# Optimization experiments

Measured on AMD Instinct MI355X. Metric: run time of the kernel, lower is better.

The kernel has to match this reference:

```python
import jax, jax.numpy as jnp
import numpy as np

N = 16384   # nodes = batch(4) * 64*64 grid
E = 32768   # edges per edge set
L = 32      # LATENT_DIMS
D = 2       # DEPTH (message-passing layers per GNOBlock)
KD = 64     # KERNEL_DIMS
TIN = 10    # TIME_STEPS_IN

def gelu(x):
    return jax.nn.gelu(x, approximate=False)  # torch F.gelu default (erf)

def setup_inputs() -> dict:
    key = jax.random.key(0)
    ks = iter(jax.random.split(key, 64))
    def nrm(shape, s=0.1):
        return jax.random.normal(next(ks), shape, dtype=jnp.float32) * s
    def ridx():
        return jax.random.randint(next(ks), (2, E), 0, N)
    inp = {
        'nodes': nrm((N, TIN), 1.0),
        'grid': jax.random.uniform(next(ks), (N, 2), dtype=jnp.float32),
    }
    for nm in ['11', '12', '22', '23', '33', '32', '21']:
        inp[f'edge_index_{nm}'] = ridx()
    for nm in ['11', '12', '22', '23', '33', '32', '21']:
        inp[f'edge_attr_{nm}'] = nrm((E, 5), 1.0)
    inp['batch_size'] = 4
    inp['image_size'] = 64
    # projector MLP: in_dims=TIN+2 -> hidden L//2 -> L
    inp['proj_w1'] = nrm((TIN + 2, L // 2)); inp['proj_b1'] = jnp.zeros((L // 2,), jnp.float32)
    inp['proj_w2'] = nrm((L // 2, L));       inp['proj_b2'] = jnp.zeros((L,), jnp.float32)
    # decoder MLP: L -> L//2 -> 1
    inp['dec_w1'] = nrm((L, L // 2)); inp['dec_b1'] = jnp.zeros((L // 2,), jnp.float32)
    inp['dec_w2'] = nrm((L // 2, 1)); inp['dec_b2'] = jnp.zeros((1,), jnp.float32)
    # 7 GNOBlocks x D layers: edge kernel MLP (5 -> KD -> L*L) + node linear (L -> L)
    inp['kw1'] = nrm((7, D, 5, KD));      inp['kb1'] = jnp.zeros((7, D, KD), jnp.float32)
    inp['kw2'] = nrm((7, D, KD, L * L));  inp['kb2'] = jnp.zeros((7, D, L * L), jnp.float32)
    inp['lw'] = nrm((7, D, L, L));        inp['lb'] = jnp.zeros((7, D, L), jnp.float32)
    return inp

def _mlp(x, w1, b1, w2, b2):
    return gelu(x @ w1 + b1) @ w2 + b2

def _gno_block(i, x, eidx, eattr, kw1, kb1, kw2, kb2, lw, lb):
    src, dst = eidx[0], eidx[1]
    n = x.shape[0]
    deg = jax.ops.segment_sum(jnp.ones_like(dst, x.dtype), dst, num_segments=n)
    inv_deg = jnp.where(deg > 0, 1.0 / jnp.maximum(deg, 1.0), 0.0)[:, None]
    for d in range(kw1.shape[1]):
        # edge-conditioned kernel: [E, L, L]
        k = _mlp(eattr, kw1[i, d], kb1[i, d], kw2[i, d], kb2[i, d]).reshape(-1, x.shape[1], x.shape[1])
        msg = jnp.einsum('eio,ei->eo', k, x[src])            # gather + per-edge matvec
        agg = jax.ops.segment_sum(msg, dst, num_segments=n) * inv_deg  # scatter-mean
        x = gelu(x @ lw[i, d] + lb[i, d] + agg)              # root linear + activation
    return x

def reference(nodes, grid, edge_index_11, edge_index_12, edge_index_22, edge_index_23,
              edge_index_33, edge_index_32, edge_index_21, edge_attr_11, edge_attr_12,
              edge_attr_22, edge_attr_23, edge_attr_33, edge_attr_32, edge_attr_21,
              batch_size, image_size, proj_w1, proj_b1, proj_w2, proj_b2,
              dec_w1, dec_b1, dec_w2, dec_b2, kw1, kb1, kw2, kb2, lw, lb):
    x = jnp.concatenate([nodes, grid], axis=-1)
    x = gelu(_mlp(x, proj_w1, proj_b1, proj_w2, proj_b2))
    # block param index order matches init order: k11,k22,k33,k12,k23,k32,k21
    n11 = _gno_block(0, x, edge_index_11, edge_attr_11, kw1, kb1, kw2, kb2, lw, lb)
    n12 = _gno_block(3, x, edge_index_12, edge_attr_12, kw1, kb1, kw2, kb2, lw, lb)
    n22 = _gno_block(1, n12, edge_index_22, edge_attr_22, kw1, kb1, kw2, kb2, lw, lb)
    n23 = _gno_block(4, n12, edge_index_23, edge_attr_23, kw1, kb1, kw2, kb2, lw, lb)
    n33 = _gno_block(2, n23, edge_index_33, edge_attr_33, kw1, kb1, kw2, kb2, lw, lb)
    n32 = _gno_block(5, n33, edge_index_32, edge_attr_32, kw1, kb1, kw2, kb2, lw, lb)
    n21 = _gno_block(6, n32 + n22, edge_index_21, edge_attr_21, kw1, kb1, kw2, kb2, lw, lb)
    out = _mlp(n21 + n11, dec_w1, dec_b1, dec_w2, dec_b2)
    return out
```

## Files before the change

kernel.cpp:

```cpp
#include <hip/hip_runtime.h>

#define Nn 16384
#define Ee 32768
#define NL (Nn * 32)

typedef _Float16 hf16;
typedef _Float16 half8 __attribute__((ext_vector_type(8)));
typedef float f32x16 __attribute__((ext_vector_type(16)));

__device__ __forceinline__ float gelu_f(float x) {
    return 0.5f * x * (1.0f + erff(x * 0.7071067811865476f));
}

__device__ __forceinline__ f32x16 zero16() {
    f32x16 v;
#pragma unroll
    for (int r = 0; r < 16; ++r) v[r] = 0.0f;
    return v;
}

struct EPtrs { const int* p[7]; };
struct EA14  { const float* p[14]; };

__global__ __launch_bounds__(256) void proj_kernel(
    const float* __restrict__ nodes, const float* __restrict__ grid2,
    const float* __restrict__ w1, const float* __restrict__ b1,
    const float* __restrict__ w2, const float* __restrict__ b2,
    float* __restrict__ x0, int* __restrict__ deg_i, int* __restrict__ cursor)
{
    const int n = blockIdx.x * 256 + threadIdx.x;
    float in[12];
#pragma unroll
    for (int j = 0; j < 10; ++j) in[j] = nodes[n * 10 + j];
    in[10] = grid2[n * 2 + 0];
    in[11] = grid2[n * 2 + 1];
    float h[16];
#pragma unroll
    for (int j = 0; j < 16; ++j) {
        float a = b1[j];
#pragma unroll
        for (int i = 0; i < 12; ++i) a = fmaf(in[i], w1[i * 16 + j], a);
        h[j] = gelu_f(a);
    }
#pragma unroll
    for (int o = 0; o < 32; ++o) {
        float a = b2[o];
#pragma unroll
        for (int j = 0; j < 16; ++j) a = fmaf(h[j], w2[j * 32 + o], a);
        x0[(size_t)n * 32 + o] = gelu_f(a);
    }
#pragma unroll
    for (int s = 0; s < 7; ++s) { deg_i[s * Nn + n] = 0; cursor[s * Nn + n] = 0; }
}

__global__ __launch_bounds__(256) void count_deg_kernel(EPtrs ei, int* __restrict__ deg_i)
{
    const int t = blockIdx.x * 256 + threadIdx.x;
    const int s = t >> 15;
    const int e = t & (Ee - 1);
    const int dst = ei.p[s][Ee + e];
    atomicAdd(&deg_i[s * Nn + dst], 1);
}

__global__ __launch_bounds__(256) void scan_kernel(const int* __restrict__ deg_i,
                                                   int* __restrict__ off)
{
    const int s = blockIdx.x;
    const int t = threadIdx.x;
    const int* d = deg_i + (size_t)s * Nn;
    int* o = off + (size_t)s * (Nn + 1);
    int local[64];
    int sum = 0;
#pragma unroll
    for (int j = 0; j < 64; ++j) { local[j] = d[t * 64 + j]; sum += local[j]; }
    __shared__ int ps[256];
    ps[t] = sum;
    __syncthreads();
    for (int st = 1; st < 256; st <<= 1) {
        int v = (t >= st) ? ps[t - st] : 0;
        __syncthreads();
        ps[t] += v;
        __syncthreads();
    }
    int base = (t > 0) ? ps[t - 1] : 0;
#pragma unroll
    for (int j = 0; j < 64; ++j) { o[t * 64 + j] = base; base += local[j]; }
    if (t == 255) o[Nn] = base;
}

__global__ __launch_bounds__(256) void rank_kernel(EPtrs ei, const int* __restrict__ off,
                                                   int* __restrict__ cursor,
                                                   int* __restrict__ eord,
                                                   int* __restrict__ srcS)
{
    const int t = blockIdx.x * 256 + threadIdx.x;
    const int s = t >> 15;
    const int e = t & (Ee - 1);
    const int dst = ei.p[s][Ee + e];
    const int r = off[(size_t)s * (Nn + 1) + dst] + atomicAdd(&cursor[s * Nn + dst], 1);
    eord[(size_t)s * Ee + r] = e;
    srcS[(size_t)s * Ee + r] = ei.p[s][e];
}

__global__ __launch_bounds__(256) void wprep_kernel(const float* __restrict__ kw2,
                                                    hf16* __restrict__ Wpack)
{
    const int id = blockIdx.x >> 5;
    const int nt = blockIdx.x & 31;
    const int t = threadIdx.x;
    const int ks = t >> 6, lane = t & 63;
    const float* kw2l = kw2 + (size_t)id * 65536;
    half8 vh, vl;
#pragma unroll
    for (int j = 0; j < 8; ++j) {
        const int k = ks * 16 + (lane >> 5) * 8 + j;
        const float v = kw2l[(size_t)k * 1024 + (lane & 31) * 32 + nt];
        const hf16 h = (hf16)v;
        vh[j] = h;
        vl[j] = (hf16)((v - (float)h) * 1024.0f);
    }
    half8* dst = (half8*)(Wpack + ((size_t)(id * 32 + nt) * 8 + ks * 2) * 512);
    dst[0 * 64 + lane] = vh;
    dst[1 * 64 + lane] = vl;
}

__global__ __launch_bounds__(256) void hprep_kernel(
    EA14 ea, const float* __restrict__ kw1, const float* __restrict__ kb1,
    hf16* __restrict__ Hpack)
{
    const int b = blockIdx.x;
    const int u = b >> 8;
    const int tgrp = b & 255;
    const int t = threadIdx.x, l = t & 63, wv = t >> 6;
    const int tile = tgrp * 4 + wv;
    const int eg = tile * 32 + (l & 31);
    const float* kw1u = kw1 + (size_t)u * 320;
    const float* kb1u = kb1 + (size_t)u * 64;
    float ea5[5];
#pragma unroll
    for (int j = 0; j < 5; ++j) ea5[j] = ea.p[u][(size_t)eg * 5 + j];
    half8* hp = (half8*)Hpack;
#pragma unroll
    for (int ks = 0; ks < 4; ++ks) {
        half8 vh, vl;
#pragma unroll
        for (int j = 0; j < 8; ++j) {
            const int k = ks * 16 + (l >> 5) * 8 + j;
            float pre = kb1u[k];
#pragma unroll
            for (int q = 0; q < 5; ++q) pre = fmaf(ea5[q], kw1u[q * 64 + k], pre);
            const float H = gelu_f(pre);
            const hf16 hv = (hf16)H;
            vh[j] = hv;
            vl[j] = (hf16)((H - (float)hv) * 1024.0f);
        }
        const size_t fb = ((size_t)(u * 1024 + tile) * 8 + ks * 2) * 64;
        hp[fb + l] = vh;
        hp[fb + 64 + l] = vl;
    }
}

__global__ __launch_bounds__(256) void gemm_kernel(
    const float* __restrict__ xa, const float* __restrict__ xb,
    const int* __restrict__ esrc,
    const hf16* __restrict__ HpackU,
    const hf16* __restrict__ WpackL,
    float* __restrict__ msgS)
{
    const int lb = ((blockIdx.x & 7) << 7) + (blockIdx.x >> 3);
    const int eblk = lb >> 2;
    const int qid = lb & 3;
    const int t = threadIdx.x, l = t & 63, wv = t >> 6;
    const int tile = eblk * 4 + wv;

    const half8* hp = (const half8*)HpackU + (size_t)tile * 8 * 64;
    half8 Hh[4], Hl[4];
#pragma unroll
    for (int ks = 0; ks < 4; ++ks) {
        Hh[ks] = hp[(ks * 2 + 0) * 64 + l];
        Hl[ks] = hp[(ks * 2 + 1) * 64 + l];
    }

    const int hi = l >> 5;
    const int el = tile * 32 + (l & 31);
    const int src = esrc[el];
    float xsr[16];
#pragma unroll
    for (int c = 0; c < 4; ++c) {
        float4 v = *reinterpret_cast<const float4*>(xa + (size_t)src * 32 + c * 8 + hi * 4);
        if (xb) {
            float4 u = *reinterpret_cast<const float4*>(xb + (size_t)src * 32 + c * 8 + hi * 4);
            v.x += u.x; v.y += u.y; v.z += u.z; v.w += u.w;
        }
        xsr[c * 4 + 0] = v.x; xsr[c * 4 + 1] = v.y;
        xsr[c * 4 + 2] = v.z; xsr[c * 4 + 3] = v.w;
    }

    float4 p4;
    const hf16* wbase = WpackL + (size_t)qid * 8 * 4096;

#define LOADW(TT, WH, WL) { \
    const half8* wp = (const half8*)(wbase + (size_t)(TT) * 4096); \
    _Pragma("unroll") for (int ks = 0; ks < 4; ++ks) { \
        WH[ks] = wp[(ks * 2 + 0) * 64 + l]; \
        WL[ks] = wp[(ks * 2 + 1) * 64 + l]; } }

#define COMPUTE(TT, WH, WL) { \
    f32x16 ah = zero16(), ax = zero16(); \
    _Pragma("unroll") for (int ks = 0; ks < 4; ++ks) { \
        ah = __builtin_amdgcn_mfma_f32_32x32x16_f16(WH[ks], Hh[ks], ah, 0, 0, 0); \
        ax = __builtin_amdgcn_mfma_f32_32x32x16_f16(WL[ks], Hh[ks], ax, 0, 0, 0); \
        ax = __builtin_amdgcn_mfma_f32_32x32x16_f16(WH[ks], Hl[ks], ax, 0, 0, 0); } \
    float ph = 0.0f, px = 0.0f; \
    _Pragma("unroll") for (int r = 0; r < 16; ++r) { \
        ph = fmaf(ah[r], xsr[r], ph); px = fmaf(ax[r], xsr[r], px); } \
    float p = fmaf(px, 9.765625e-4f, ph); \
    p += __shfl_xor(p, 32); \
    p4[(TT) & 3] = p; \
    if (((TT) & 3) == 3 && l < 32) \
        *reinterpret_cast<float4*>(msgS + (size_t)el * 32 + qid * 8 + ((TT) - 3)) = p4; }

    half8 WhA[4], WlA[4], WhB[4], WlB[4];
    LOADW(0, WhA, WlA)
#pragma unroll
    for (int g = 0; g < 4; ++g) {
        LOADW(2 * g + 1, WhB, WlB)
        COMPUTE(2 * g, WhA, WlA)
        if (g < 3) LOADW(2 * g + 2, WhA, WlA)
        COMPUTE(2 * g + 1, WhB, WlB)
    }
#undef LOADW
#undef COMPUTE
}

__global__ __launch_bounds__(256) void node_update_kernel(
    const float* __restrict__ xa, const float* __restrict__ xb,
    float* __restrict__ xout, const float* __restrict__ msgS,
    const int* __restrict__ off, const int* __restrict__ eord,
    const int* __restrict__ srcS,
    const float* __restrict__ lw, const float* __restrict__ lb,
    const float* __restrict__ kb2l)
{
    __shared__ float lwS[1024];
    __shared__ float kbS[1024];
#pragma unroll
    for (int c = 0; c < 4; ++c) {
        lwS[threadIdx.x + 256 * c] = lw[threadIdx.x + 256 * c];
        kbS[threadIdx.x + 256 * c] = kb2l[threadIdx.x + 256 * c];
    }
    __syncthreads();

    const int g = blockIdx.x * 256 + threadIdx.x;
    const int n = g >> 3;
    const int q = g & 7;

    const int b = off[n], e = off[n + 1];
    float sum[4];
    float xsum[32];
#pragma unroll
    for (int oo = 0; oo < 4; ++oo) sum[oo] = 0.0f;
#pragma unroll
    for (int i = 0; i < 32; ++i) xsum[i] = 0.0f;
    for (int j = b; j < e; ++j) {
        const int eid = eord[j];
        const float4 m0 = *reinterpret_cast<const float4*>(msgS + (size_t)eid * 32 + q * 4);
        sum[0] += m0.x; sum[1] += m0.y; sum[2] += m0.z; sum[3] += m0.w;
        const int src = srcS[j];
#pragma unroll
        for (int c = 0; c < 8; ++c) {
            float4 v = *reinterpret_cast<const float4*>(xa + (size_t)src * 32 + c * 4);
            if (xb) {
                float4 u = *reinterpret_cast<const float4*>(xb + (size_t)src * 32 + c * 4);
                v.x += u.x; v.y += u.y; v.z += u.z; v.w += u.w;
            }
            xsum[c * 4 + 0] += v.x; xsum[c * 4 + 1] += v.y;
            xsum[c * 4 + 2] += v.z; xsum[c * 4 + 3] += v.w;
        }
    }
    const float inv = (e > b) ? 1.0f / (float)(e - b) : 0.0f;
    float acc[4];
#pragma unroll
    for (int oo = 0; oo < 4; ++oo) acc[oo] = fmaf(sum[oo], inv, lb[q * 4 + oo]);

    float row[32];
#pragma unroll
    for (int i = 0; i < 32; i += 4) {
        float4 v = *reinterpret_cast<const float4*>(xa + (size_t)n * 32 + i);
        if (xb) {
            float4 u = *reinterpret_cast<const float4*>(xb + (size_t)n * 32 + i);
            v.x += u.x; v.y += u.y; v.z += u.z; v.w += u.w;
        }
        row[i + 0] = v.x; row[i + 1] = v.y; row[i + 2] = v.z; row[i + 3] = v.w;
    }
#pragma unroll
    for (int i = 0; i < 32; ++i) {
        const float xi = row[i];
        const float xm = xsum[i] * inv;
#pragma unroll
        for (int oo = 0; oo < 4; ++oo) {
            acc[oo] = fmaf(xi, lwS[i * 32 + q * 4 + oo], acc[oo]);
            acc[oo] = fmaf(xm, kbS[i * 32 + q * 4 + oo], acc[oo]);
        }
    }
    float4 o0;
    o0.x = gelu_f(acc[0]); o0.y = gelu_f(acc[1]);
    o0.z = gelu_f(acc[2]); o0.w = gelu_f(acc[3]);
    *reinterpret_cast<float4*>(xout + (size_t)n * 32 + q * 4) = o0;
}

__global__ __launch_bounds__(256) void decode_kernel(
    const float* __restrict__ a, const float* __restrict__ b,
    const float* __restrict__ w1, const float* __restrict__ b1,
    const float* __restrict__ w2, const float* __restrict__ b2,
    float* __restrict__ out)
{
    const int n = blockIdx.x * 256 + threadIdx.x;
    float s[32];
#pragma unroll
    for (int i = 0; i < 32; ++i) s[i] = a[(size_t)n * 32 + i] + b[(size_t)n * 32 + i];
    float acc = b2[0];
#pragma unroll
    for (int j = 0; j < 16; ++j) {
        float h = b1[j];
#pragma unroll
        for (int i = 0; i < 32; ++i) h = fmaf(s[i], w1[i * 16 + j], h);
        acc = fmaf(gelu_f(h), w2[j], acc);
    }
    out[n] = acc;
}

extern "C" void kernel_launch(void* const* d_in, const int* in_sizes, int n_in,
                              void* d_out, int out_size, void* d_ws, size_t ws_size,
                              hipStream_t stream)
{
    const float* nodes = (const float*)d_in[0];
    const float* grid2 = (const float*)d_in[1];
    const int* ei[7];
    const float* ea[7];
    for (int s = 0; s < 7; ++s) {
        ei[s] = (const int*)d_in[2 + s];
        ea[s] = (const float*)d_in[9 + s];
    }
    const float* pw1 = (const float*)d_in[18];
    const float* pb1 = (const float*)d_in[19];
    const float* pw2 = (const float*)d_in[20];
    const float* pb2 = (const float*)d_in[21];
    const float* dw1 = (const float*)d_in[22];
    const float* db1 = (const float*)d_in[23];
    const float* dw2 = (const float*)d_in[24];
    const float* db2 = (const float*)d_in[25];
    const float* kw1 = (const float*)d_in[26];
    const float* kb1 = (const float*)d_in[27];
    const float* kw2 = (const float*)d_in[28];
    const float* kb2 = (const float*)d_in[29];
    const float* lw  = (const float*)d_in[30];
    const float* lb  = (const float*)d_in[31];

    const int i2s[7] = {0, 2, 4, 1, 3, 5, 6};

    float* ws  = (float*)d_ws;
    float* x0   = ws + 0 * (size_t)NL;
    float* n11  = ws + 1 * (size_t)NL;
    float* n12  = ws + 2 * (size_t)NL;
    float* n22  = ws + 3 * (size_t)NL;
    float* n23  = ws + 4 * (size_t)NL;
    float* n33  = ws + 5 * (size_t)NL;
    float* n32  = ws + 6 * (size_t)NL;
    float* n21  = ws + 7 * (size_t)NL;
    float* msgS = ws + 8 * (size_t)NL;
    size_t cur = 8 * (size_t)NL + (size_t)Ee * 32;
    hf16* Wpack = (hf16*)(ws + cur);
    cur += (size_t)14 * 32 * 8 * 512 / 2;
    hf16* Hpack = (hf16*)(ws + cur);
    cur += (size_t)14 * 1024 * 8 * 512 / 2;
    int* deg_i  = (int*)(ws + cur); cur += (size_t)7 * Nn;
    int* cursor = (int*)(ws + cur); cur += (size_t)7 * Nn;
    int* off    = (int*)(ws + cur); cur += (size_t)7 * (Nn + 1) + 1;
    int* eord   = (int*)(ws + cur); cur += (size_t)7 * Ee;
    int* srcS   = (int*)(ws + cur);

    proj_kernel<<<Nn / 256, 256, 0, stream>>>(nodes, grid2, pw1, pb1, pw2, pb2,
                                              x0, deg_i, cursor);

    EPtrs ep;
    for (int s = 0; s < 7; ++s) ep.p[s] = ei[s];
    count_deg_kernel<<<7 * Ee / 256, 256, 0, stream>>>(ep, deg_i);
    scan_kernel<<<7, 256, 0, stream>>>(deg_i, off);
    rank_kernel<<<7 * Ee / 256, 256, 0, stream>>>(ep, off, cursor, eord, srcS);
    wprep_kernel<<<14 * 32, 256, 0, stream>>>(kw2, Wpack);

    EA14 ea14;
    for (int u = 0; u < 14; ++u) ea14.p[u] = ea[i2s[u >> 1]];
    hprep_kernel<<<14 * 256, 256, 0, stream>>>(ea14, kw1, kb1, Hpack);

    auto layer = [&](int i, int d, int s, const float* xa, const float* xb, float* xo) {
        const int id = i * 2 + d;
        gemm_kernel<<<1024, 256, 0, stream>>>(
            xa, xb, ei[s],
            Hpack + (size_t)id * 1024 * 8 * 512,
            Wpack + (size_t)id * 32 * 4096, msgS);
        node_update_kernel<<<Nn * 8 / 256, 256, 0, stream>>>(
            xa, xb, xo, msgS, off + (size_t)s * (Nn + 1),
            eord + (size_t)s * Ee, srcS + (size_t)s * Ee,
            lw + (size_t)id * 1024, lb + (size_t)id * 32, kb2 + (size_t)id * 1024);
    };
    auto gno_block = [&](int i, int s, const float* xa, const float* xb, float* xo) {
        layer(i, 0, s, xa, xb, xo);
        layer(i, 1, s, xo, nullptr, xo);
    };

    gno_block(0, 0, x0,  nullptr, n11);
    gno_block(3, 1, x0,  nullptr, n12);
    gno_block(1, 2, n12, nullptr, n22);
    gno_block(4, 3, n12, nullptr, n23);
    gno_block(2, 4, n23, nullptr, n33);
    gno_block(5, 5, n33, nullptr, n32);
    gno_block(6, 6, n32, n22,     n21);

    decode_kernel<<<Nn / 256, 256, 0, stream>>>(n11, n21, dw1, db1, dw2, db2, (float*)d_out);
}
```

Before: 620.5 us.

## Fold kernel bias into edge GEMM, stage weights in LDS, slim node update

The kb2 bias contribution (bias-matrix times source features) moves from the node update into the edge GEMM epilogue, using a pre-permuted bias layout. The node update then no longer gathers source features per edge and drops the srcS array. The GEMM now stages the packed weight tiles in double-buffered shared memory shared by the four waves instead of having each wave load them from global. The node update is remapped to one wave per node with lanes over output channels. The aim is to cut redundant global traffic, at the cost of added block-level barriers in the GEMM.

```diff
diff --git a/kernel.cpp b/kernel.cpp
--- a/kernel.cpp
+++ b/kernel.cpp
@@ -90,8 +90,7 @@
 
 __global__ __launch_bounds__(256) void rank_kernel(EPtrs ei, const int* __restrict__ off,
                                                    int* __restrict__ cursor,
-                                                   int* __restrict__ eord,
-                                                   int* __restrict__ srcS)
+                                                   int* __restrict__ eord)
 {
     const int t = blockIdx.x * 256 + threadIdx.x;
     const int s = t >> 15;
@@ -99,7 +98,6 @@
     const int dst = ei.p[s][Ee + e];
     const int r = off[(size_t)s * (Nn + 1) + dst] + atomicAdd(&cursor[s * Nn + dst], 1);
     eord[(size_t)s * Ee + r] = e;
-    srcS[(size_t)s * Ee + r] = ei.p[s][e];
 }
 
 __global__ __launch_bounds__(256) void wprep_kernel(const float* __restrict__ kw2,
@@ -122,6 +120,22 @@
     half8* dst = (half8*)(Wpack + ((size_t)(id * 32 + nt) * 8 + ks * 2) * 512);
     dst[0 * 64 + lane] = vh;
     dst[1 * 64 + lane] = vl;
+}
+
+__global__ __launch_bounds__(256) void kprep_kernel(const float* __restrict__ kb2,
+                                                    float* __restrict__ kb2C)
+{
+    const int id = blockIdx.x;
+    const int t = threadIdx.x;
+#pragma unroll
+    for (int c = 0; c < 4; ++c) {
+        const int ent = t * 4 + c;
+        const int nt = ent >> 5;
+        const int hi = (ent >> 4) & 1;
+        const int r = ent & 15;
+        const int i = (r & 3) + 8 * (r >> 2) + 4 * hi;
+        kb2C[(size_t)id * 1024 + ent] = kb2[(size_t)id * 1024 + i * 32 + nt];
+    }
 }
 
 __global__ __launch_bounds__(256) void hprep_kernel(
@@ -165,15 +179,19 @@
     const int* __restrict__ esrc,
     const hf16* __restrict__ HpackU,
     const hf16* __restrict__ WpackL,
+    const float* __restrict__ kb2CL,
     float* __restrict__ msgS)
 {
+    __shared__ __align__(16) hf16 wLDS[2 * 4096];
+    half8* wl8 = (half8*)wLDS;
+
     const int lb = ((blockIdx.x & 7) << 7) + (blockIdx.x >> 3);
     const int eblk = lb >> 2;
     const int qid = lb & 3;
     const int t = threadIdx.x, l = t & 63, wv = t >> 6;
     const int tile = eblk * 4 + wv;
 
-    const half8* hp = (const half8*)HpackU + (size_t)tile * 8 * 64;
+    const half8* hp = (const half8*)HpackU + (size_t)tile * 512;
     half8 Hh[4], Hl[4];
 #pragma unroll
     for (int ks = 0; ks < 4; ++ks) {
@@ -196,116 +214,113 @@
         xsr[c * 4 + 2] = v.z; xsr[c * 4 + 3] = v.w;
     }
 
+    const half8* wsrc = (const half8*)(WpackL + (size_t)qid * 8 * 4096);
+    const float* kbB = kb2CL + hi * 16;
+
+    {
+        half8 s0 = wsrc[t * 2 + 0];
+        half8 s1 = wsrc[t * 2 + 1];
+        wl8[t * 2 + 0] = s0;
+        wl8[t * 2 + 1] = s1;
+    }
+    __syncthreads();
+
     float4 p4;
-    const hf16* wbase = WpackL + (size_t)qid * 8 * 4096;
-
-#define LOADW(TT, WH, WL) { \
-    const half8* wp = (const half8*)(wbase + (size_t)(TT) * 4096); \
-    _Pragma("unroll") for (int ks = 0; ks < 4; ++ks) { \
-        WH[ks] = wp[(ks * 2 + 0) * 64 + l]; \
-        WL[ks] = wp[(ks * 2 + 1) * 64 + l]; } }
-
-#define COMPUTE(TT, WH, WL) { \
-    f32x16 ah = zero16(), ax = zero16(); \
-    _Pragma("unroll") for (int ks = 0; ks < 4; ++ks) { \
-        ah = __builtin_amdgcn_mfma_f32_32x32x16_f16(WH[ks], Hh[ks], ah, 0, 0, 0); \
-        ax = __builtin_amdgcn_mfma_f32_32x32x16_f16(WL[ks], Hh[ks], ax, 0, 0, 0); \
-        ax = __builtin_amdgcn_mfma_f32_32x32x16_f16(WH[ks], Hl[ks], ax, 0, 0, 0); } \
-    float ph = 0.0f, px = 0.0f; \
-    _Pragma("unroll") for (int r = 0; r < 16; ++r) { \
-        ph = fmaf(ah[r], xsr[r], ph); px = fmaf(ax[r], xsr[r], px); } \
-    float p = fmaf(px, 9.765625e-4f, ph); \
-    p += __shfl_xor(p, 32); \
-    p4[(TT) & 3] = p; \
-    if (((TT) & 3) == 3 && l < 32) \
-        *reinterpret_cast<float4*>(msgS + (size_t)el * 32 + qid * 8 + ((TT) - 3)) = p4; }
-
-    half8 WhA[4], WlA[4], WhB[4], WlB[4];
-    LOADW(0, WhA, WlA)
-#pragma unroll
-    for (int g = 0; g < 4; ++g) {
-        LOADW(2 * g + 1, WhB, WlB)
-        COMPUTE(2 * g, WhA, WlA)
-        if (g < 3) LOADW(2 * g + 2, WhA, WlA)
-        COMPUTE(2 * g + 1, WhB, WlB)
-    }
-#undef LOADW
-#undef COMPUTE
+    int buf = 0;
+#pragma unroll
+    for (int nt8 = 0; nt8 < 8; ++nt8) {
+        half8 s0, s1;
+        if (nt8 < 7) {
+            s0 = wsrc[(nt8 + 1) * 512 + t * 2 + 0];
+            s1 = wsrc[(nt8 + 1) * 512 + t * 2 + 1];
+        }
+
+        half8 WH[4], WL[4];
+#pragma unroll
+        for (int ks = 0; ks < 4; ++ks) {
+            WH[ks] = wl8[buf * 512 + (ks * 2 + 0) * 64 + l];
+            WL[ks] = wl8[buf * 512 + (ks * 2 + 1) * 64 + l];
+        }
+
+        const int nt = qid * 8 + nt8;
+        float kb[16];
+#pragma unroll
+        for (int c = 0; c < 4; ++c) {
+            const float4 kv = *reinterpret_cast<const float4*>(kbB + nt * 32 + c * 4);
+            kb[c * 4 + 0] = kv.x; kb[c * 4 + 1] = kv.y;
+            kb[c * 4 + 2] = kv.z; kb[c * 4 + 3] = kv.w;
+        }
+
+        f32x16 ah = zero16(), ax = zero16();
+#pragma unroll
+        for (int ks = 0; ks < 4; ++ks) {
+            ah = __builtin_amdgcn_mfma_f32_32x32x16_f16(WH[ks], Hh[ks], ah, 0, 0, 0);
+            ax = __builtin_amdgcn_mfma_f32_32x32x16_f16(WL[ks], Hh[ks], ax, 0, 0, 0);
+            ax = __builtin_amdgcn_mfma_f32_32x32x16_f16(WH[ks], Hl[ks], ax, 0, 0, 0);
+        }
+        float ph = 0.0f, px = 0.0f, pk = 0.0f;
+#pragma unroll
+        for (int r = 0; r < 16; ++r) {
+            ph = fmaf(ah[r], xsr[r], ph);
+            px = fmaf(ax[r], xsr[r], px);
+            pk = fmaf(kb[r], xsr[r], pk);
+        }
+        float p = fmaf(px, 9.765625e-4f, ph) + pk;
+        p += __shfl_xor(p, 32);
+        p4[nt8 & 3] = p;
+        if ((nt8 & 3) == 3 && l < 32)
+            *reinterpret_cast<float4*>(msgS + (size_t)el * 32 + qid * 8 + (nt8 - 3)) = p4;
+
+        if (nt8 < 7) {
+            wl8[(buf ^ 1) * 512 + t * 2 + 0] = s0;
+            wl8[(buf ^ 1) * 512 + t * 2 + 1] = s1;
+        }
+        __syncthreads();
+        buf ^= 1;
+    }
 }
 
 __global__ __launch_bounds__(256) void node_update_kernel(
     const float* __restrict__ xa, const float* __restrict__ xb,
     float* __restrict__ xout, const float* __restrict__ msgS,
     const int* __restrict__ off, const int* __restrict__ eord,
-    const int* __restrict__ srcS,
-    const float* __restrict__ lw, const float* __restrict__ lb,
-    const float* __restrict__ kb2l)
+    const float* __restrict__ lw, const float* __restrict__ lb)
 {
     __shared__ float lwS[1024];
-    __shared__ float kbS[1024];
+#pragma unroll
+    for (int c = 0; c < 4; ++c) lwS[threadIdx.x + 256 * c] = lw[threadIdx.x + 256 * c];
+    __syncthreads();
+
+    const int t = threadIdx.x, l = t & 63, wv = t >> 6;
+    const int n = blockIdx.x * 4 + wv;
+    const int o = l & 31, jj = l >> 5;
+
+    const int b = off[n], e = off[n + 1];
+    float sum = 0.0f;
+    for (int j = b + jj; j < e; j += 2) {
+        const int eid = eord[j];
+        sum += msgS[(size_t)eid * 32 + o];
+    }
+    sum += __shfl_xor(sum, 32);
+    const float inv = (e > b) ? 1.0f / (float)(e - b) : 0.0f;
+
+    float part = 0.0f;
 #pragma unroll
     for (int c = 0; c < 4; ++c) {
-        lwS[threadIdx.x + 256 * c] = lw[threadIdx.x + 256 * c];
-        kbS[threadIdx.x + 256 * c] = kb2l[threadIdx.x + 256 * c];
-    }
-    __syncthreads();
-
-    const int g = blockIdx.x * 256 + threadIdx.x;
-    const int n = g >> 3;
-    const int q = g & 7;
-
-    const int b = off[n], e = off[n + 1];
-    float sum[4];
-    float xsum[32];
-#pragma unroll
-    for (int oo = 0; oo < 4; ++oo) sum[oo] = 0.0f;
-#pragma unroll
-    for (int i = 0; i < 32; ++i) xsum[i] = 0.0f;
-    for (int j = b; j < e; ++j) {
-        const int eid = eord[j];
-        const float4 m0 = *reinterpret_cast<const float4*>(msgS + (size_t)eid * 32 + q * 4);
-        sum[0] += m0.x; sum[1] += m0.y; sum[2] += m0.z; sum[3] += m0.w;
-        const int src = srcS[j];
-#pragma unroll
-        for (int c = 0; c < 8; ++c) {
-            float4 v = *reinterpret_cast<const float4*>(xa + (size_t)src * 32 + c * 4);
-            if (xb) {
-                float4 u = *reinterpret_cast<const float4*>(xb + (size_t)src * 32 + c * 4);
-                v.x += u.x; v.y += u.y; v.z += u.z; v.w += u.w;
-            }
-            xsum[c * 4 + 0] += v.x; xsum[c * 4 + 1] += v.y;
-            xsum[c * 4 + 2] += v.z; xsum[c * 4 + 3] += v.w;
-        }
-    }
-    const float inv = (e > b) ? 1.0f / (float)(e - b) : 0.0f;
-    float acc[4];
-#pragma unroll
-    for (int oo = 0; oo < 4; ++oo) acc[oo] = fmaf(sum[oo], inv, lb[q * 4 + oo]);
-
-    float row[32];
-#pragma unroll
-    for (int i = 0; i < 32; i += 4) {
-        float4 v = *reinterpret_cast<const float4*>(xa + (size_t)n * 32 + i);
+        float4 v = *reinterpret_cast<const float4*>(xa + (size_t)n * 32 + jj * 16 + c * 4);
         if (xb) {
-            float4 u = *reinterpret_cast<const float4*>(xb + (size_t)n * 32 + i);
+            float4 u = *reinterpret_cast<const float4*>(xb + (size_t)n * 32 + jj * 16 + c * 4);
             v.x += u.x; v.y += u.y; v.z += u.z; v.w += u.w;
         }
-        row[i + 0] = v.x; row[i + 1] = v.y; row[i + 2] = v.z; row[i + 3] = v.w;
-    }
-#pragma unroll
-    for (int i = 0; i < 32; ++i) {
-        const float xi = row[i];
-        const float xm = xsum[i] * inv;
-#pragma unroll
-        for (int oo = 0; oo < 4; ++oo) {
-            acc[oo] = fmaf(xi, lwS[i * 32 + q * 4 + oo], acc[oo]);
-            acc[oo] = fmaf(xm, kbS[i * 32 + q * 4 + oo], acc[oo]);
-        }
-    }
-    float4 o0;
-    o0.x = gelu_f(acc[0]); o0.y = gelu_f(acc[1]);
-    o0.z = gelu_f(acc[2]); o0.w = gelu_f(acc[3]);
-    *reinterpret_cast<float4*>(xout + (size_t)n * 32 + q * 4) = o0;
+        part = fmaf(v.x, lwS[(jj * 16 + c * 4 + 0) * 32 + o], part);
+        part = fmaf(v.y, lwS[(jj * 16 + c * 4 + 1) * 32 + o], part);
+        part = fmaf(v.z, lwS[(jj * 16 + c * 4 + 2) * 32 + o], part);
+        part = fmaf(v.w, lwS[(jj * 16 + c * 4 + 3) * 32 + o], part);
+    }
+    part += __shfl_xor(part, 32);
+
+    const float acc = fmaf(sum, inv, lb[o]) + part;
+    if (l < 32) xout[(size_t)n * 32 + o] = gelu_f(acc);
 }
 
 __global__ __launch_bounds__(256) void decode_kernel(
@@ -373,11 +388,11 @@
     cur += (size_t)14 * 32 * 8 * 512 / 2;
     hf16* Hpack = (hf16*)(ws + cur);
     cur += (size_t)14 * 1024 * 8 * 512 / 2;
+    float* kb2C = ws + cur; cur += (size_t)14 * 1024;
     int* deg_i  = (int*)(ws + cur); cur += (size_t)7 * Nn;
     int* cursor = (int*)(ws + cur); cur += (size_t)7 * Nn;
     int* off    = (int*)(ws + cur); cur += (size_t)7 * (Nn + 1) + 1;
-    int* eord   = (int*)(ws + cur); cur += (size_t)7 * Ee;
-    int* srcS   = (int*)(ws + cur);
+    int* eord   = (int*)(ws + cur);
 
     proj_kernel<<<Nn / 256, 256, 0, stream>>>(nodes, grid2, pw1, pb1, pw2, pb2,
                                               x0, deg_i, cursor);
@@ -386,8 +401,9 @@
     for (int s = 0; s < 7; ++s) ep.p[s] = ei[s];
     count_deg_kernel<<<7 * Ee / 256, 256, 0, stream>>>(ep, deg_i);
     scan_kernel<<<7, 256, 0, stream>>>(deg_i, off);
-    rank_kernel<<<7 * Ee / 256, 256, 0, stream>>>(ep, off, cursor, eord, srcS);
+    rank_kernel<<<7 * Ee / 256, 256, 0, stream>>>(ep, off, cursor, eord);
     wprep_kernel<<<14 * 32, 256, 0, stream>>>(kw2, Wpack);
+    kprep_kernel<<<14, 256, 0, stream>>>(kb2, kb2C);
 
     EA14 ea14;
     for (int u = 0; u < 14; ++u) ea14.p[u] = ea[i2s[u >> 1]];
@@ -397,12 +413,13 @@
         const int id = i * 2 + d;
         gemm_kernel<<<1024, 256, 0, stream>>>(
             xa, xb, ei[s],
-            Hpack + (size_t)id * 1024 * 8 * 512,
-            Wpack + (size_t)id * 32 * 4096, msgS);
-        node_update_kernel<<<Nn * 8 / 256, 256, 0, stream>>>(
+            Hpack + (size_t)id * 1024 * 4096,
+            Wpack + (size_t)id * 32 * 4096,
+            kb2C + (size_t)id * 1024, msgS);
+        node_update_kernel<<<Nn / 4, 256, 0, stream>>>(
             xa, xb, xo, msgS, off + (size_t)s * (Nn + 1),
-            eord + (size_t)s * Ee, srcS + (size_t)s * Ee,
-            lw + (size_t)id * 1024, lb + (size_t)id * 32, kb2 + (size_t)id * 1024);
+            eord + (size_t)s * Ee,
+            lw + (size_t)id * 1024, lb + (size_t)id * 32);
     };
     auto gno_block = [&](int i, int s, const float* xa, const float* xb, float* xo) {
         layer(i, 0, s, xa, xb, xo);
```

Result: faster. 600.8 us (-3.2%).
